# Kernel tuning notes

Measured on AMD Instinct MI355X. Metric: run time of the kernel, lower is better.

Reference implementation:

```python
import jax, jax.numpy as jnp
import numpy as np

CHAMPION_COUNT = 170
N_NODES = 500_000
NODES_PER_GRAPH = 10
N_GRAPHS = N_NODES // NODES_PER_GRAPH
N_EDGES = 4_000_000
CH_DIM, ROLE_DIM, HID = 32, 8, 64
NODE_DIM = CH_DIM + ROLE_DIM + 1  # 41
EPS = 1e-5


def setup_inputs() -> dict:
    key = jax.random.key(0)
    ks = jax.random.split(key, 20)
    # node features: [champ_id, role_id, team_id]
    champ = jax.random.randint(ks[0], (N_NODES,), 0, CHAMPION_COUNT)
    role = jax.random.randint(ks[1], (N_NODES,), 0, 10)
    team = jax.random.randint(ks[2], (N_NODES,), 0, 2)
    x = jnp.stack([champ, role, team], axis=1).astype(jnp.int64)
    # intra-graph random edges (10-node match graphs)
    ge = jax.random.randint(ks[3], (N_EDGES,), 0, N_GRAPHS)
    src = ge * NODES_PER_GRAPH + jax.random.randint(ks[4], (N_EDGES,), 0, NODES_PER_GRAPH)
    dst = ge * NODES_PER_GRAPH + jax.random.randint(ks[5], (N_EDGES,), 0, NODES_PER_GRAPH)
    edge_index = jnp.stack([src, dst], axis=0).astype(jnp.int64)
    batch = (jnp.arange(N_NODES) // NODES_PER_GRAPH).astype(jnp.int64)
    f32 = jnp.float32
    return {
        "x": x, "edge_index": edge_index, "batch": batch,
        "champ_table": jax.random.normal(ks[6], (CHAMPION_COUNT, CH_DIM), f32),
        "role_table": jax.random.normal(ks[7], (10, ROLE_DIM), f32),
        "W1": jax.random.normal(ks[8], (NODE_DIM, HID), f32) * (1.0 / np.sqrt(NODE_DIM)),
        "b1": jnp.zeros((HID,), f32),
        "gamma1": jnp.ones((HID,), f32), "beta1": jnp.zeros((HID,), f32),
        "W2": jax.random.normal(ks[9], (HID, HID), f32) * (1.0 / np.sqrt(HID)),
        "b2": jnp.zeros((HID,), f32),
        "fc1_W": jax.random.normal(ks[10], (HID, HID // 2), f32) * (1.0 / np.sqrt(HID)),
        "fc1_b": jnp.zeros((HID // 2,), f32),
        "gamma2": jnp.ones((HID // 2,), f32), "beta2": jnp.zeros((HID // 2,), f32),
        "fc2_W": jax.random.normal(ks[11], (HID // 2, 1), f32) * (1.0 / np.sqrt(HID // 2)),
        "fc2_b": jnp.zeros((1,), f32),
    }


def gcn_conv(h, W, b, src, dst, n_nodes):
    # PyG GCNConv: add self loops, symmetric degree normalization, then scatter-add.
    hw = h @ W                                             # [N, out]
    deg = jnp.zeros((n_nodes,), hw.dtype).at[dst].add(1.0) + 1.0  # +1 self loop
    dinv = jax.lax.rsqrt(deg)
    norm = dinv[src] * dinv[dst]                           # [E]
    agg = jnp.zeros_like(hw).at[dst].add(norm[:, None] * hw[src])
    agg = agg + (dinv * dinv)[:, None] * hw                # self-loop messages
    return agg + b


def batchnorm(h, gamma, beta):
    mu = jnp.mean(h, axis=0)
    var = jnp.mean(jnp.square(h - mu), axis=0)  # biased var, as torch BN
    return (h - mu) * jax.lax.rsqrt(var + EPS) * gamma + beta


def reference(x, edge_index, batch, champ_table, role_table, W1, b1, gamma1, beta1,
              W2, b2, fc1_W, fc1_b, gamma2, beta2, fc2_W, fc2_b):
    src, dst = edge_index[0], edge_index[1]
    h = jnp.concatenate([
        champ_table[x[:, 0]],
        role_table[x[:, 1]],
        x[:, 2:3].astype(champ_table.dtype),
    ], axis=1)                                             # [N, 41]
    h = jax.nn.relu(batchnorm(gcn_conv(h, W1, b1, src, dst, N_NODES), gamma1, beta1))
    h = jax.nn.relu(gcn_conv(h, W2, b2, src, dst, N_NODES))  # dropout = identity (eval)
    # global mean pool over graphs
    sums = jax.ops.segment_sum(h, batch, num_segments=N_GRAPHS)
    cnts = jax.ops.segment_sum(jnp.ones((h.shape[0],), h.dtype), batch, num_segments=N_GRAPHS)
    g = sums / jnp.maximum(cnts, 1.0)[:, None]             # [G, 64]
    g = jax.nn.relu(batchnorm(g @ fc1_W + fc1_b, gamma2, beta2))
    return jax.nn.sigmoid(g @ fc2_W + fc2_b)               # [G, 1]
```

## Files before the change

kernel.cpp:

```cpp
#include <hip/hip_runtime.h>
#include <hip/hip_bf16.h>
#include <math.h>

typedef __attribute__((ext_vector_type(8))) short bf16x8;
typedef __attribute__((ext_vector_type(4))) float f32x4;

#define N_NODES   500000
#define N_GRAPHS  50000
#define N_EDGES   4000000
#define NPB   4000
#define NB    391
#define BCAP  12288

#define REC_OFF   0u
#define ZB_OFF    0u
#define G_OFF     6400000u
#define TAIL_OFF  19218432u
#define P1S_OFF   19220000u
#define P1Q_OFF   19252768u
#define P2S_OFF   19285536u
#define P2Q_OFF   19301920u
#define ZERO_LEN  99872u
#define CHW_OFF   19318304u
#define ROW_OFF   19361824u
#define W2F_OFF   19364384u
#define F1F_OFF   19380768u
#define SC_OFF    19388960u
#define WM_OFF    19389728u

__device__ __forceinline__ void split8v(const float v[8], bf16x8 &h, bf16x8 &l) {
    #pragma unroll
    for (int e = 0; e < 8; e++) {
        __hip_bfloat16 hb = __float2bfloat16(v[e]);
        float hf = __bfloat162float(hb);
        __hip_bfloat16 lb = __float2bfloat16(v[e] - hf);
        h[e] = __builtin_bit_cast(short, hb);
        l[e] = __builtin_bit_cast(short, lb);
    }
}

__global__ __launch_bounds__(256) void k_tabfrag(
    const float* __restrict__ champ, const float* __restrict__ role,
    const float* __restrict__ W1, const float* __restrict__ W2,
    const float* __restrict__ fc1W,
    float* __restrict__ chW, float* __restrict__ roW,
    bf16x8* __restrict__ w2f, bf16x8* __restrict__ f1f)
{
    if (blockIdx.x < 45) {
        int t = blockIdx.x * 256 + threadIdx.x;
        if (t < 170 * 64) {
            int c = t >> 6, j = t & 63;
            float s = 0.f;
            #pragma unroll
            for (int k = 0; k < 32; k++) s += champ[c * 32 + k] * W1[k * 64 + j];
            chW[t] = s;
        } else {
            int t2 = t - 170 * 64;
            int r = t2 >> 6, j = t2 & 63;
            float s = 0.f;
            #pragma unroll
            for (int k = 0; k < 8; k++) s += role[r * 8 + k] * W1[(32 + k) * 64 + j];
            roW[t2] = s;
        }
    } else if (threadIdx.x < 64) {
        const int lane = threadIdx.x, q = lane >> 4, c = lane & 15;
        #pragma unroll
        for (int ks = 0; ks < 2; ks++)
        #pragma unroll
        for (int t = 0; t < 4; t++) {
            float v[8];
            #pragma unroll
            for (int e = 0; e < 8; e++) {
                int k = 32 * ks + (e < 4 ? 4 * q + e : 16 + 4 * q + (e - 4));
                v[e] = W2[k * 64 + 16 * t + c];
            }
            bf16x8 h, l; split8v(v, h, l);
            w2f[(ks * 4 + t) * 64 + lane] = h;
            w2f[(8 + ks * 4 + t) * 64 + lane] = l;
        }
        #pragma unroll
        for (int ks = 0; ks < 2; ks++)
        #pragma unroll
        for (int t = 0; t < 2; t++) {
            float v[8];
            #pragma unroll
            for (int e = 0; e < 8; e++) {
                int k = 32 * ks + (e < 4 ? 4 * q + e : 16 + 4 * q + (e - 4));
                v[e] = fc1W[k * 32 + 16 * t + c];
            }
            bf16x8 h, l; split8v(v, h, l);
            f1f[(ks * 2 + t) * 64 + lane] = h;
            f1f[(4 + ks * 2 + t) * 64 + lane] = l;
        }
    }
}

__global__ __launch_bounds__(256) void k_part(const int* __restrict__ ei,
                                              unsigned* __restrict__ rec,
                                              unsigned* __restrict__ tail) {
    __shared__ unsigned lcnt[NB];
    __shared__ unsigned gbase[NB];
    const int tid = threadIdx.x;
    const int e0 = blockIdx.x * NPB;

    for (int i = tid; i < NB; i += 256) lcnt[i] = 0;
    __syncthreads();
    for (int i = tid; i < NPB; i += 256) {
        unsigned d = (unsigned)ei[N_EDGES + e0 + i];
        atomicAdd(&lcnt[d / 1280u], 1u);
    }
    __syncthreads();
    for (int b = tid; b < NB; b += 256) {
        unsigned c = lcnt[b];
        gbase[b] = (unsigned)b * BCAP + (c ? atomicAdd(&tail[b], c) : 0u);
    }
    __syncthreads();
    for (int i = tid; i < NB; i += 256) lcnt[i] = 0;
    __syncthreads();
    for (int i = tid; i < NPB; i += 256) {
        unsigned s = (unsigned)ei[e0 + i];
        unsigned d = (unsigned)ei[N_EDGES + e0 + i];
        unsigned g = d / 10u;
        unsigned key = g * 100u + (d - g * 10u) * 10u + (s % 10u);
        unsigned b = g >> 7;
        unsigned pos = gbase[b] + atomicAdd(&lcnt[b], 1u);
        rec[pos] = key;
    }
}

__global__ __launch_bounds__(256) void k_count(const unsigned* __restrict__ rec,
                                               const unsigned* __restrict__ tail,
                                               float* __restrict__ wmat) {
    __shared__ unsigned cw[128 * 25];
    const int tid = threadIdx.x;
    const unsigned b = blockIdx.x;

    for (int i = tid; i < 3200; i += 256) cw[i] = 0;
    __syncthreads();
    const unsigned n = tail[b];
    const unsigned base = b * BCAP;
    for (unsigned i = tid; i < n; i += 256) {
        unsigned key = rec[base + i];
        unsigned g = key / 100u;
        unsigned slot = key - g * 100u;
        atomicAdd(&cw[(g & 127u) * 25u + (slot >> 2)], 1u << (8u * (slot & 3u)));
    }
    __syncthreads();
    if (tid < 128) {
        unsigned g = b * 128u + (unsigned)tid;
        if (g < N_GRAPHS) {
            float c100[100];
            #pragma unroll
            for (int i = 0; i < 25; i++) {
                unsigned w = cw[tid * 25 + i];
                c100[4 * i + 0] = (float)(w & 255u);
                c100[4 * i + 1] = (float)((w >> 8) & 255u);
                c100[4 * i + 2] = (float)((w >> 16) & 255u);
                c100[4 * i + 3] = (float)(w >> 24);
            }
            float dinv[10];
            #pragma unroll
            for (int u = 0; u < 10; u++) {
                float s = 1.f;
                #pragma unroll
                for (int v = 0; v < 10; v++) s += c100[u * 10 + v];
                dinv[u] = rsqrtf(s);
            }
            #pragma unroll
            for (int u = 0; u < 10; u++)
                #pragma unroll
                for (int v = 0; v < 10; v++)
                    c100[u * 10 + v] = (c100[u * 10 + v] + (u == v ? 1.f : 0.f)) * dinv[u] * dinv[v];
            float4* wp = (float4*)(wmat + (size_t)g * 100);
            #pragma unroll
            for (int r = 0; r < 25; r++)
                wp[r] = make_float4(c100[4 * r], c100[4 * r + 1], c100[4 * r + 2], c100[4 * r + 3]);
        }
    }
}

__global__ __launch_bounds__(256) void k_pass1(
    const int* __restrict__ x, const float* __restrict__ wmat,
    const float* __restrict__ chW, const float* __restrict__ roW,
    const float* __restrict__ W1, const float* __restrict__ b1,
    float* __restrict__ p1s, float* __restrict__ p1q)
{
    const int lane = threadIdx.x & 63;
    const int g = __builtin_amdgcn_readfirstlane(blockIdx.x * 4 + (threadIdx.x >> 6));
    const int* xg = x + g * 30;
    const float* wm = wmat + g * 100;

    const float w1t = W1[40 * 64 + lane];
    float hw[10];
    #pragma unroll
    for (int u = 0; u < 10; u++) {
        int cu = xg[u * 3 + 0];
        int ru = xg[u * 3 + 1];
        float tm = (float)xg[u * 3 + 2];
        hw[u] = chW[cu * 64 + lane] + roW[ru * 64 + lane] + tm * w1t;
    }
    const float b1v = b1[lane];
    float s = 0.f, ss = 0.f;
    #pragma unroll
    for (int u = 0; u < 10; u++) {
        float a = b1v;
        #pragma unroll
        for (int v = 0; v < 10; v++) a = fmaf(wm[u * 10 + v], hw[v], a);
        s += a; ss += a * a;
    }
    int slot = g & 127;
    atomicAdd(&p1s[slot * 64 + lane], s);
    atomicAdd(&p1q[slot * 64 + lane], ss);
}

__global__ __launch_bounds__(1024) void k_fin1(
    const float* __restrict__ p1s, const float* __restrict__ p1q,
    const float* __restrict__ gamma, const float* __restrict__ beta,
    float* __restrict__ sc)
{
    __shared__ double rs[16][64], rq[16][64];
    int s = threadIdx.x >> 6, j = threadIdx.x & 63;
    double a = 0.0, b = 0.0;
    for (int k = s; k < 128; k += 16) { a += p1s[k * 64 + j]; b += p1q[k * 64 + j]; }
    rs[s][j] = a; rq[s][j] = b;
    __syncthreads();
    if (s == 0) {
        for (int k = 1; k < 16; k++) { a += rs[k][j]; b += rq[k][j]; }
        double mu = a / (double)N_NODES;
        double var = b / (double)N_NODES - mu * mu;
        float scl = gamma[j] * rsqrtf((float)var + 1e-5f);
        sc[j] = scl;
        sc[64 + j] = beta[j] - (float)mu * scl;
    }
}

__global__ __launch_bounds__(256) void k_main(
    const int* __restrict__ x, const float* __restrict__ wmat,
    const float* __restrict__ chW, const float* __restrict__ roW,
    const float* __restrict__ W1, const float* __restrict__ b1,
    const float* __restrict__ sc,
    const bf16x8* __restrict__ w2f, const float* __restrict__ b2,
    float* __restrict__ G)
{
    __shared__ float stage[4][1088];

    const int w = threadIdx.x >> 6, lane = threadIdx.x & 63;
    const int q = lane >> 4, c = lane & 15;
    const int wid = __builtin_amdgcn_readfirstlane((int)blockIdx.x * 4 + w);

    float* up = stage[w];
    for (int i = lane; i < 408; i += 64) up[680 + i] = 0.f;

    const float w1t = W1[40 * 64 + lane];
    const float b1v = b1[lane];
    const float sc1 = sc[lane], sf1 = sc[64 + lane];
    float b2v[4];
    #pragma unroll
    for (int t = 0; t < 4; t++) b2v[t] = b2[16 * t + c];

    #pragma unroll 1
    for (int gi = 0; gi < 4; gi++) {
        const int g = wid * 4 + gi;
        const int* xg = x + g * 30;
        const float* wm = wmat + g * 100;

        float hw[10];
        #pragma unroll
        for (int u = 0; u < 10; u++) {
            int cu = xg[u * 3 + 0];
            int ru = xg[u * 3 + 1];
            float tm = (float)xg[u * 3 + 2];
            hw[u] = chW[cu * 64 + lane] + roW[ru * 64 + lane] + tm * w1t;
        }
        float h1[10];
        #pragma unroll
        for (int u = 0; u < 10; u++) {
            float a = b1v;
            #pragma unroll
            for (int v2 = 0; v2 < 10; v2++) a = fmaf(wm[u * 10 + v2], hw[v2], a);
            h1[u] = fmaxf(fmaf(a, sc1, sf1), 0.f);
        }
        #pragma unroll
        for (int u = 0; u < 10; u++) {
            float t = 0.f;
            #pragma unroll
            for (int v2 = 0; v2 < 10; v2++) t = fmaf(wm[u * 10 + v2], h1[v2], t);
            up[u * 68 + lane] = t;
        }
        f32x4 acc[4] = {f32x4{0.f,0.f,0.f,0.f}, f32x4{0.f,0.f,0.f,0.f},
                        f32x4{0.f,0.f,0.f,0.f}, f32x4{0.f,0.f,0.f,0.f}};
        const float4* rowp = (const float4*)(up + c * 68);
        #pragma unroll
        for (int ks = 0; ks < 2; ks++) {
            float4 A0 = rowp[8 * ks + q];
            float4 A1 = rowp[8 * ks + 4 + q];
            float av[8] = {A0.x, A0.y, A0.z, A0.w, A1.x, A1.y, A1.z, A1.w};
            bf16x8 ah, al; split8v(av, ah, al);
            #pragma unroll
            for (int t = 0; t < 4; t++) {
                bf16x8 bh = w2f[(ks * 4 + t) * 64 + lane];
                bf16x8 bl = w2f[(8 + ks * 4 + t) * 64 + lane];
                acc[t] = __builtin_amdgcn_mfma_f32_16x16x32_bf16(ah, bh, acc[t], 0, 0, 0);
                acc[t] = __builtin_amdgcn_mfma_f32_16x16x32_bf16(al, bh, acc[t], 0, 0, 0);
                acc[t] = __builtin_amdgcn_mfma_f32_16x16x32_bf16(ah, bl, acc[t], 0, 0, 0);
            }
        }
        float pool[4];
        #pragma unroll
        for (int t = 0; t < 4; t++) {
            float pt = 0.f;
            #pragma unroll
            for (int r = 0; r < 4; r++) {
                int m = 4 * q + r;
                float val = fmaxf(acc[t][r] + b2v[t], 0.f);
                pt += (m < 10) ? val : 0.f;
            }
            pt += __shfl_xor(pt, 16);
            pt += __shfl_xor(pt, 32);
            pool[t] = pt * 0.1f;
        }
        float gv = (q == 0) ? pool[0] : (q == 1) ? pool[1] : (q == 2) ? pool[2] : pool[3];
        G[(size_t)g * 64 + lane] = gv;
    }
}

__global__ __launch_bounds__(256) void k_fc(
    const float* __restrict__ G, const bf16x8* __restrict__ f1f,
    const float* __restrict__ fc1b,
    float* __restrict__ zbuf, float* __restrict__ p2s, float* __restrict__ p2q)
{
    const int w = threadIdx.x >> 6, lane = threadIdx.x & 63;
    const int q = lane >> 4, c = lane & 15;
    const int wid = __builtin_amdgcn_readfirstlane((int)blockIdx.x * 4 + w);
    if (wid >= N_GRAPHS / 16) return;
    const int g0 = wid * 16;

    float f1bv[2];
    #pragma unroll
    for (int t = 0; t < 2; t++) f1bv[t] = fc1b[16 * t + c];

    f32x4 facc[2] = {f32x4{0.f,0.f,0.f,0.f}, f32x4{0.f,0.f,0.f,0.f}};
    const float* grow = G + (size_t)(g0 + c) * 64;
    #pragma unroll
    for (int ks = 0; ks < 2; ks++) {
        float4 G0 = *(const float4*)(grow + 32 * ks + 4 * q);
        float4 G1 = *(const float4*)(grow + 32 * ks + 16 + 4 * q);
        float gvv[8] = {G0.x, G0.y, G0.z, G0.w, G1.x, G1.y, G1.z, G1.w};
        bf16x8 gh, gl; split8v(gvv, gh, gl);
        #pragma unroll
        for (int t = 0; t < 2; t++) {
            bf16x8 fh = f1f[(ks * 2 + t) * 64 + lane];
            bf16x8 fl = f1f[(4 + ks * 2 + t) * 64 + lane];
            facc[t] = __builtin_amdgcn_mfma_f32_16x16x32_bf16(gh, fh, facc[t], 0, 0, 0);
            facc[t] = __builtin_amdgcn_mfma_f32_16x16x32_bf16(gl, fh, facc[t], 0, 0, 0);
            facc[t] = __builtin_amdgcn_mfma_f32_16x16x32_bf16(gh, fl, facc[t], 0, 0, 0);
        }
    }
    #pragma unroll
    for (int t = 0; t < 2; t++)
    #pragma unroll
    for (int r = 0; r < 4; r++) {
        int gg = g0 + 4 * q + r;
        float zv = facc[t][r] + f1bv[t];
        zbuf[gg * 32 + 16 * t + c] = zv;
        int slot = gg & 127;
        atomicAdd(&p2s[slot * 32 + 16 * t + c], zv);
        atomicAdd(&p2q[slot * 32 + 16 * t + c], zv * zv);
    }
}

__global__ __launch_bounds__(512) void k_fin2(
    const float* __restrict__ p2s, const float* __restrict__ p2q,
    const float* __restrict__ gamma, const float* __restrict__ beta,
    float* __restrict__ sc)
{
    __shared__ double rs[16][32], rq[16][32];
    int s = threadIdx.x >> 5, j = threadIdx.x & 31;
    double a = 0.0, b = 0.0;
    for (int k = s; k < 128; k += 16) { a += p2s[k * 32 + j]; b += p2q[k * 32 + j]; }
    rs[s][j] = a; rq[s][j] = b;
    __syncthreads();
    if (s == 0) {
        for (int k = 1; k < 16; k++) { a += rs[k][j]; b += rq[k][j]; }
        double mu = a / (double)N_GRAPHS;
        double var = b / (double)N_GRAPHS - mu * mu;
        float scl = gamma[j] * rsqrtf((float)var + 1e-5f);
        sc[128 + j] = scl;
        sc[160 + j] = beta[j] - (float)mu * scl;
    }
}

__global__ __launch_bounds__(256) void k_pass3(
    const float* __restrict__ z, const float* __restrict__ sc,
    const float* __restrict__ fc2W, const float* __restrict__ fc2b,
    float* __restrict__ out)
{
    int t = blockIdx.x * blockDim.x + threadIdx.x;
    int g = t >> 5, j = t & 31;
    float y = fmaxf(fmaf(z[g * 32 + j], sc[128 + j], sc[160 + j]), 0.f);
    float acc = y * fc2W[j];
    #pragma unroll
    for (int off = 16; off > 0; off >>= 1) acc += __shfl_xor(acc, off, 32);
    if (j == 0) out[g] = 1.0f / (1.0f + __expf(-(acc + fc2b[0])));
}

extern "C" void kernel_launch(void* const* d_in, const int* in_sizes, int n_in,
                              void* d_out, int out_size, void* d_ws, size_t ws_size,
                              hipStream_t stream) {
    const int*   x      = (const int*)d_in[0];
    const int*   ei     = (const int*)d_in[1];
    const float* champ  = (const float*)d_in[3];
    const float* role   = (const float*)d_in[4];
    const float* W1     = (const float*)d_in[5];
    const float* b1     = (const float*)d_in[6];
    const float* gamma1 = (const float*)d_in[7];
    const float* beta1  = (const float*)d_in[8];
    const float* W2     = (const float*)d_in[9];
    const float* b2     = (const float*)d_in[10];
    const float* fc1W   = (const float*)d_in[11];
    const float* fc1b   = (const float*)d_in[12];
    const float* gamma2 = (const float*)d_in[13];
    const float* beta2  = (const float*)d_in[14];
    const float* fc2W   = (const float*)d_in[15];
    const float* fc2b   = (const float*)d_in[16];
    float* out = (float*)d_out;

    char* ws = (char*)d_ws;
    unsigned* rec  = (unsigned*)(ws + REC_OFF);
    unsigned* tail = (unsigned*)(ws + TAIL_OFF);
    float* zbuf = (float*)(ws + ZB_OFF);
    float* G    = (float*)(ws + G_OFF);
    float* p1s  = (float*)(ws + P1S_OFF);
    float* p1q  = (float*)(ws + P1Q_OFF);
    float* p2s  = (float*)(ws + P2S_OFF);
    float* p2q  = (float*)(ws + P2Q_OFF);
    float* chW  = (float*)(ws + CHW_OFF);
    float* roW  = (float*)(ws + ROW_OFF);
    bf16x8* w2f = (bf16x8*)(ws + W2F_OFF);
    bf16x8* f1f = (bf16x8*)(ws + F1F_OFF);
    float* scb  = (float*)(ws + SC_OFF);
    float* wmat = (float*)(ws + WM_OFF);

    hipMemsetAsync(ws + TAIL_OFF, 0, ZERO_LEN, stream);
    k_tabfrag<<<46, 256, 0, stream>>>(champ, role, W1, W2, fc1W, chW, roW, w2f, f1f);
    k_part<<<N_EDGES / NPB, 256, 0, stream>>>(ei, rec, tail);
    k_count<<<NB, 256, 0, stream>>>(rec, tail, wmat);
    k_pass1<<<N_GRAPHS / 4, 256, 0, stream>>>(x, wmat, chW, roW, W1, b1, p1s, p1q);
    k_fin1<<<1, 1024, 0, stream>>>(p1s, p1q, gamma1, beta1, scb);
    k_main<<<N_GRAPHS / 16, 256, 0, stream>>>(x, wmat, chW, roW, W1, b1, scb,
                                              w2f, b2, G);
    k_fc<<<(N_GRAPHS / 16 + 3) / 4, 256, 0, stream>>>(G, f1f, fc1b, zbuf, p2s, p2q);
    k_fin2<<<1, 512, 0, stream>>>(p2s, p2q, gamma2, beta2, scb);
    k_pass3<<<N_GRAPHS / 8, 256, 0, stream>>>(zbuf, scb, fc2W, fc2b, out);
}
```

Before: 325.9 us.

## Stage edge partition through shared-memory bucket sort for coalesced record writes

The edge partition kernel now uses larger chunks of 16384 edges and 512-thread blocks. It computes per-bucket local offsets with a wavefront prefix scan and scatters keys into a shared-memory sorted array first. It then writes each bucket's run contiguously to global memory, so global stores land in runs instead of scattered single words. This costs 64KB+ of LDS per block, which limits occupancy, and there are fewer blocks (245) to keep the GPU busy.

```diff
diff --git a/kernel.cpp b/kernel.cpp
--- a/kernel.cpp
+++ b/kernel.cpp
@@ -8,7 +8,8 @@
 #define N_NODES   500000
 #define N_GRAPHS  50000
 #define N_EDGES   4000000
-#define NPB   4000
+#define NPB   16384
+#define NPART ((N_EDGES + NPB - 1) / NPB)
 #define NB    391
 #define BCAP  12288
 
@@ -95,36 +96,64 @@
     }
 }
 
-__global__ __launch_bounds__(256) void k_part(const int* __restrict__ ei,
+__global__ __launch_bounds__(512) void k_part(const int* __restrict__ ei,
                                               unsigned* __restrict__ rec,
                                               unsigned* __restrict__ tail) {
-    __shared__ unsigned lcnt[NB];
+    __shared__ unsigned hist[NB];
+    __shared__ unsigned lofs[NB];
     __shared__ unsigned gbase[NB];
+    __shared__ unsigned sorted[NPB];
     const int tid = threadIdx.x;
     const int e0 = blockIdx.x * NPB;
-
-    for (int i = tid; i < NB; i += 256) lcnt[i] = 0;
-    __syncthreads();
-    for (int i = tid; i < NPB; i += 256) {
+    const int n = min(NPB, N_EDGES - e0);
+
+    for (int i = tid; i < NB; i += 512) hist[i] = 0;
+    __syncthreads();
+    for (int i = tid; i < n; i += 512) {
         unsigned d = (unsigned)ei[N_EDGES + e0 + i];
-        atomicAdd(&lcnt[d / 1280u], 1u);
-    }
-    __syncthreads();
-    for (int b = tid; b < NB; b += 256) {
-        unsigned c = lcnt[b];
+        atomicAdd(&hist[d / 1280u], 1u);
+    }
+    __syncthreads();
+    if (tid < 64) {
+        unsigned part = 0;
+        #pragma unroll
+        for (int j = 0; j < 7; j++) {
+            int b = tid * 7 + j;
+            if (b < NB) part += hist[b];
+        }
+        unsigned scan = part;
+        #pragma unroll
+        for (int off = 1; off < 64; off <<= 1) {
+            unsigned t = __shfl_up(scan, off, 64);
+            if (tid >= off) scan += t;
+        }
+        unsigned excl = scan - part;
+        #pragma unroll
+        for (int j = 0; j < 7; j++) {
+            int b = tid * 7 + j;
+            if (b < NB) { unsigned h = hist[b]; lofs[b] = excl; excl += h; }
+        }
+    }
+    __syncthreads();
+    for (int b = tid; b < NB; b += 512) {
+        unsigned c = hist[b];
         gbase[b] = (unsigned)b * BCAP + (c ? atomicAdd(&tail[b], c) : 0u);
-    }
-    __syncthreads();
-    for (int i = tid; i < NB; i += 256) lcnt[i] = 0;
-    __syncthreads();
-    for (int i = tid; i < NPB; i += 256) {
+        hist[b] = lofs[b];
+    }
+    __syncthreads();
+    for (int i = tid; i < n; i += 512) {
         unsigned s = (unsigned)ei[e0 + i];
         unsigned d = (unsigned)ei[N_EDGES + e0 + i];
         unsigned g = d / 10u;
         unsigned key = g * 100u + (d - g * 10u) * 10u + (s % 10u);
-        unsigned b = g >> 7;
-        unsigned pos = gbase[b] + atomicAdd(&lcnt[b], 1u);
-        rec[pos] = key;
+        unsigned pos = atomicAdd(&hist[g >> 7], 1u);
+        sorted[pos] = key;
+    }
+    __syncthreads();
+    for (int i = tid; i < n; i += 512) {
+        unsigned key = sorted[i];
+        unsigned b = (key / 100u) >> 7;
+        rec[gbase[b] + ((unsigned)i - lofs[b])] = key;
     }
 }
 
@@ -443,7 +472,7 @@
 
     hipMemsetAsync(ws + TAIL_OFF, 0, ZERO_LEN, stream);
     k_tabfrag<<<46, 256, 0, stream>>>(champ, role, W1, W2, fc1W, chW, roW, w2f, f1f);
-    k_part<<<N_EDGES / NPB, 256, 0, stream>>>(ei, rec, tail);
+    k_part<<<NPART, 512, 0, stream>>>(ei, rec, tail);
     k_count<<<NB, 256, 0, stream>>>(rec, tail, wmat);
     k_pass1<<<N_GRAPHS / 4, 256, 0, stream>>>(x, wmat, chW, roW, W1, b1, p1s, p1q);
     k_fin1<<<1, 1024, 0, stream>>>(p1s, p1q, gamma1, beta1, scb);
```

Measured after the change: 293.0 us. 1.11x faster.
